# Kernel optimization log

Hardware: AMD Instinct MI355X
Metric: run time of the kernel (lower is better)

## Reference

```python
import jax, jax.numpy as jnp
import numpy as np
from jax.scipy.linalg import cho_solve

N_OBS = 2_000_000
DIM = 16
EPS = 1e-6
LOG_DIM = 32  # module uses self.dim = 32 (param count) in the log-2pi term; faithful to source


def _block_diag_cov(params):
    # params: (32,) -> 8 blocks of 2x2, block = B @ B^T + eps*I, assembled block-diagonally
    B = params.reshape(8, 2, 2)
    blocks = jnp.einsum('nij,nkj->nik', B, B) + EPS * jnp.eye(2, dtype=params.dtype)
    idx = jnp.arange(8)
    M = jnp.zeros((8, 2, 8, 2), dtype=params.dtype).at[idx, :, idx, :].set(blocks)
    return M.reshape(16, 16)


def _transform_mu(mu, pose):
    # interleaved (x,y) points, rotate about centroid, translate to pose[:2]
    pts = jnp.stack([mu[0::2], mu[1::2]])  # (2, 8)
    centroid = jnp.mean(pts, axis=1, keepdims=True)
    ct, st = jnp.cos(pose[2]), jnp.sin(pose[2])
    R = jnp.stack([jnp.stack([ct, -st]), jnp.stack([st, ct])])  # (2,2)
    pts = R @ (pts - centroid) + pose[:2, None]
    return jnp.zeros(16, dtype=mu.dtype).at[0::2].set(pts[0]).at[1::2].set(pts[1])


def setup_inputs() -> dict:
    key = jax.random.key(0)
    k1, k2, k3, k4, k5 = jax.random.split(key, 5)
    obs = jax.random.normal(k1, (N_OBS, DIM), dtype=jnp.float32)
    mu_likelihood = jax.random.normal(k2, (DIM,), dtype=jnp.float32)
    # pose init ~ [uniform(15,25), uniform(15,25), uniform(-pi/16, pi/16)]
    u = jax.random.uniform(k3, (3,), dtype=jnp.float32)
    mu_prior_pose = jnp.array([15.0, 15.0, -np.pi / 16], jnp.float32) + u * jnp.array([10.0, 10.0, 2 * np.pi / 16], jnp.float32)
    # covariance params ~ uniform(cov_min=0.01, cov_max=10)
    Sigma_prior_params = jax.random.uniform(k4, (32,), dtype=jnp.float32, minval=0.01, maxval=10.0)
    Sigma_likelihood_params = jax.random.uniform(k5, (32,), dtype=jnp.float32, minval=0.01, maxval=10.0)
    return {
        'obs': obs,
        'mu_likelihood': mu_likelihood,
        'mu_prior_pose': mu_prior_pose,
        'Sigma_prior_params': Sigma_prior_params,
        'Sigma_likelihood_params': Sigma_likelihood_params,
    }


def reference(obs, mu_likelihood, mu_prior_pose, Sigma_prior_params, Sigma_likelihood_params):
    Sigma_prior = _block_diag_cov(Sigma_prior_params)
    Sigma_likelihood = _block_diag_cov(Sigma_likelihood_params)
    eye = jnp.eye(DIM, dtype=jnp.float32)

    L_prior = jnp.linalg.cholesky(Sigma_prior)
    prior_precision = cho_solve((L_prior, True), eye)
    L_like = jnp.linalg.cholesky(Sigma_likelihood)
    like_precision = cho_solve((L_like, True), eye)

    posterior_precision = prior_precision + like_precision
    L_post = jnp.linalg.cholesky(posterior_precision)
    Sigma_post = cho_solve((L_post, True), eye)

    mu_prior = _transform_mu(mu_likelihood, mu_prior_pose)
    mu_post = Sigma_post @ (cho_solve((L_prior, True), mu_prior) + cho_solve((L_like, True), mu_likelihood))

    diff = obs - mu_post  # (N, 16)
    # NOTE: faithful to source, which uses logdet of the *precision* and
    # quad form with Sigma_post = inv(posterior_precision)
    logdet = 2.0 * jnp.sum(jnp.log(jnp.diagonal(L_post)))
    quad = jnp.sum((diff @ Sigma_post) * diff, axis=1)  # (N,)
    log_terms = -0.5 * LOG_DIM * jnp.log(jnp.asarray(2.0 * jnp.pi, jnp.float32)) - 0.5 * logdet - 0.5 * quad
    return -jnp.sum(log_terms)
```

## Files before the change

### kernel.cpp

```cpp
#include <hip/hip_runtime.h>
#include <math.h>

#define EPS_COV 1e-6f
#define NBLOCKS 2048

typedef float vfloat4 __attribute__((ext_vector_type(4)));


__global__ __launch_bounds__(256) void quad_stream_kernel(
    const vfloat4* __restrict__ obs4,
    const float*  __restrict__ mu_like,
    const float*  __restrict__ pose,
    const float*  __restrict__ sp_prior,
    const float*  __restrict__ sp_like,
    double*       __restrict__ partials,
    int n4)
{
    const int tid    = blockIdx.x * blockDim.x + threadIdx.x;
    const int stride = gridDim.x * blockDim.x;
    const int q = tid & 3;

    float cx = 0.f, cy = 0.f;
    #pragma unroll
    for (int i = 0; i < 8; ++i) { cx += mu_like[2*i]; cy += mu_like[2*i+1]; }
    cx *= 0.125f; cy *= 0.125f;
    const float ct = cosf(pose[2]), st = sinf(pose[2]);
    const float tx = pose[0], ty = pose[1];

    float m0=0.f, m1=0.f, m2=0.f, m3=0.f;
    float a0=0.f, b0=0.f, c0=0.f, a1=0.f, b1=0.f, c1=0.f;

    #pragma unroll
    for (int n = 0; n < 8; ++n) {
        float px = mu_like[2*n]   - cx;
        float py = mu_like[2*n+1] - cy;
        float mp0 = ct*px - st*py + tx;
        float mp1 = st*px + ct*py + ty;

        const float* p = sp_prior + 4*n;
        float s00 = p[0]*p[0] + p[1]*p[1] + EPS_COV;
        float s01 = p[0]*p[2] + p[1]*p[3];
        float s11 = p[2]*p[2] + p[3]*p[3] + EPS_COV;
        float det = s00*s11 - s01*s01;
        float Pp00 =  s11/det, Pp01 = -s01/det, Pp11 = s00/det;

        const float* l = sp_like + 4*n;
        float t00 = l[0]*l[0] + l[1]*l[1] + EPS_COV;
        float t01 = l[0]*l[2] + l[1]*l[3];
        float t11 = l[2]*l[2] + l[3]*l[3] + EPS_COV;
        float dl = t00*t11 - t01*t01;
        float Pl00 =  t11/dl, Pl01 = -t01/dl, Pl11 = t00/dl;

        float Q00 = Pp00 + Pl00, Q01 = Pp01 + Pl01, Q11 = Pp11 + Pl11;
        float dq = Q00*Q11 - Q01*Q01;
        float S00 = Q11/dq, S01 = -Q01/dq, S11v = Q00/dq;

        float ml0 = mu_like[2*n], ml1 = mu_like[2*n+1];
        float v0 = Pp00*mp0 + Pp01*mp1 + Pl00*ml0 + Pl01*ml1;
        float v1 = Pp01*mp0 + Pp11*mp1 + Pl01*ml0 + Pl11*ml1;
        float mpostx = S00*v0 + S01*v1;
        float mposty = S01*v0 + S11v*v1;

        if (n == 2*q)     { m0 = mpostx; m1 = mposty; a0 = S00; b0 = 2.f*S01; c0 = S11v; }
        if (n == 2*q + 1) { m2 = mpostx; m3 = mposty; a1 = S00; b1 = 2.f*S01; c1 = S11v; }
    }

    float acc0 = 0.f, acc1 = 0.f;
    int i = tid;
    while (i + 7*stride < n4) {
        vfloat4 v[8];
        #pragma unroll
        for (int j = 0; j < 8; ++j)
            v[j] = __builtin_nontemporal_load(&obs4[i + j*stride]);
        #pragma unroll
        for (int j = 0; j < 8; ++j) {
            float d0 = v[j].x - m0, d1 = v[j].y - m1;
            float d2 = v[j].z - m2, d3 = v[j].w - m3;
            float t = a0*d0*d0 + b0*(d0*d1) + c0*d1*d1
                    + a1*d2*d2 + b1*(d2*d3) + c1*d3*d3;
            if (j & 1) acc1 += t; else acc0 += t;
        }
        i += 8*stride;
    }
    for (; i < n4; i += stride) {
        vfloat4 v = __builtin_nontemporal_load(&obs4[i]);
        float d0 = v.x - m0, d1 = v.y - m1;
        float d2 = v.z - m2, d3 = v.w - m3;
        acc0 += a0*d0*d0 + b0*(d0*d1) + c0*d1*d1
              + a1*d2*d2 + b1*(d2*d3) + c1*d3*d3;
    }

    double accd = (double)acc0 + (double)acc1;

    #pragma unroll
    for (int off = 32; off > 0; off >>= 1)
        accd += __shfl_down(accd, off, 64);

    __shared__ double lds[4];
    const int wave = threadIdx.x >> 6;
    if ((threadIdx.x & 63) == 0) lds[wave] = accd;
    __syncthreads();
    if (threadIdx.x == 0)
        partials[blockIdx.x] = lds[0] + lds[1] + lds[2] + lds[3];
}

__global__ __launch_bounds__(256) void finalize_kernel(
    const double* __restrict__ partials,
    const float*  __restrict__ sp_prior,
    const float*  __restrict__ sp_like,
    float*        __restrict__ out,
    int nblocks, double n_obs)
{
    double s = 0.0;
    for (int i = threadIdx.x; i < nblocks; i += 256) s += partials[i];
    #pragma unroll
    for (int off = 32; off > 0; off >>= 1)
        s += __shfl_down(s, off, 64);
    __shared__ double lds[4];
    const int wave = threadIdx.x >> 6;
    if ((threadIdx.x & 63) == 0) lds[wave] = s;
    __syncthreads();

    if (threadIdx.x == 0) {
        double total = lds[0] + lds[1] + lds[2] + lds[3];
        double logdet = 0.0;
        for (int n = 0; n < 8; ++n) {
            const float* p = sp_prior + 4*n;
            double s00 = (double)p[0]*p[0] + (double)p[1]*p[1] + 1e-6;
            double s01 = (double)p[0]*p[2] + (double)p[1]*p[3];
            double s11 = (double)p[2]*p[2] + (double)p[3]*p[3] + 1e-6;
            double det = s00*s11 - s01*s01;
            double Pp00 = s11/det, Pp01 = -s01/det, Pp11 = s00/det;
            const float* l = sp_like + 4*n;
            double t00 = (double)l[0]*l[0] + (double)l[1]*l[1] + 1e-6;
            double t01 = (double)l[0]*l[2] + (double)l[1]*l[3];
            double t11 = (double)l[2]*l[2] + (double)l[3]*l[3] + 1e-6;
            double dl = t00*t11 - t01*t01;
            double Pl00 = t11/dl, Pl01 = -t01/dl, Pl11 = t00/dl;
            double Q00 = Pp00 + Pl00, Q01 = Pp01 + Pl01, Q11 = Pp11 + Pl11;
            logdet += log(Q00*Q11 - Q01*Q01);
        }
        const double LOG_2PI = 1.8378770664093454835606594728112;
        double c = n_obs * (16.0 * LOG_2PI + 0.5 * logdet);
        out[0] = (float)(c + 0.5 * total);
    }
}

extern "C" void kernel_launch(void* const* d_in, const int* in_sizes, int n_in,
                              void* d_out, int out_size, void* d_ws, size_t ws_size,
                              hipStream_t stream) {
    const float* obs      = (const float*)d_in[0];
    const float* mu_like  = (const float*)d_in[1];
    const float* pose     = (const float*)d_in[2];
    const float* sp_prior = (const float*)d_in[3];
    const float* sp_like  = (const float*)d_in[4];
    float* out = (float*)d_out;

    double* partials = (double*)d_ws;

    const int n_elems  = in_sizes[0];
    const int n4       = n_elems / 4;
    const double n_obs = (double)(n_elems / 16);

    quad_stream_kernel<<<NBLOCKS, 256, 0, stream>>>(
        (const vfloat4*)obs, mu_like, pose, sp_prior, sp_like, partials, n4);

    finalize_kernel<<<1, 256, 0, stream>>>(partials, sp_prior, sp_like, out, NBLOCKS, n_obs);
}
```

Baseline: 194.3 us.

## Fuse streaming reduction and finalize into one cooperative kernel with grid sync

```diff
diff --git a/kernel.cpp b/kernel.cpp
--- a/kernel.cpp
+++ b/kernel.cpp
@@ -1,69 +1,109 @@
 #include <hip/hip_runtime.h>
+#include <hip/hip_cooperative_groups.h>
 #include <math.h>
 
+namespace cg = cooperative_groups;
+
 #define EPS_COV 1e-6f
-#define NBLOCKS 2048
+#define NBLOCKS 1024
+#define NTHREADS 256
 
 typedef float vfloat4 __attribute__((ext_vector_type(4)));
 
 
-__global__ __launch_bounds__(256) void quad_stream_kernel(
+
+__device__ __forceinline__ void setup_params(
+    const float* __restrict__ mu_like, const float* __restrict__ pose,
+    const float* __restrict__ sp_prior, const float* __restrict__ sp_like, int q,
+    float& m0, float& m1, float& m2, float& m3,
+    float& a0, float& b0, float& c0,
+    float& a1, float& b1, float& c1)
+{
+    float cx = 0.f, cy = 0.f;
+    #pragma unroll
+    for (int i = 0; i < 8; ++i) { cx += mu_like[2*i]; cy += mu_like[2*i+1]; }
+    cx *= 0.125f; cy *= 0.125f;
+    const float ct = cosf(pose[2]), st = sinf(pose[2]);
+    const float tx = pose[0], ty = pose[1];
+
+    #pragma unroll
+    for (int k = 0; k < 2; ++k) {
+        const int n = 2*q + k;
+        float px = mu_like[2*n]   - cx;
+        float py = mu_like[2*n+1] - cy;
+        float mp0 = ct*px - st*py + tx;
+        float mp1 = st*px + ct*py + ty;
+
+        const float* p = sp_prior + 4*n;
+        float s00 = p[0]*p[0] + p[1]*p[1] + EPS_COV;
+        float s01 = p[0]*p[2] + p[1]*p[3];
+        float s11 = p[2]*p[2] + p[3]*p[3] + EPS_COV;
+        float det = s00*s11 - s01*s01;
+        float Pp00 =  s11/det, Pp01 = -s01/det, Pp11 = s00/det;
+
+        const float* l = sp_like + 4*n;
+        float t00 = l[0]*l[0] + l[1]*l[1] + EPS_COV;
+        float t01 = l[0]*l[2] + l[1]*l[3];
+        float t11 = l[2]*l[2] + l[3]*l[3] + EPS_COV;
+        float dl = t00*t11 - t01*t01;
+        float Pl00 =  t11/dl, Pl01 = -t01/dl, Pl11 = t00/dl;
+
+        float Q00 = Pp00 + Pl00, Q01 = Pp01 + Pl01, Q11 = Pp11 + Pl11;
+        float dq = Q00*Q11 - Q01*Q01;
+        float S00 = Q11/dq, S01 = -Q01/dq, S11v = Q00/dq;
+
+        float ml0 = mu_like[2*n], ml1 = mu_like[2*n+1];
+        float v0 = Pp00*mp0 + Pp01*mp1 + Pl00*ml0 + Pl01*ml1;
+        float v1 = Pp01*mp0 + Pp11*mp1 + Pl01*ml0 + Pl11*ml1;
+        float mpostx = S00*v0 + S01*v1;
+        float mposty = S01*v0 + S11v*v1;
+
+        if (k == 0) { m0 = mpostx; m1 = mposty; a0 = S00; b0 = 2.f*S01; c0 = S11v; }
+        else        { m2 = mpostx; m3 = mposty; a1 = S00; b1 = 2.f*S01; c1 = S11v; }
+    }
+}
+
+__device__ __forceinline__ double logdet_posterior(
+    const float* __restrict__ sp_prior, const float* __restrict__ sp_like)
+{
+    double logdet = 0.0;
+    for (int n = 0; n < 8; ++n) {
+        const float* p = sp_prior + 4*n;
+        double s00 = (double)p[0]*p[0] + (double)p[1]*p[1] + 1e-6;
+        double s01 = (double)p[0]*p[2] + (double)p[1]*p[3];
+        double s11 = (double)p[2]*p[2] + (double)p[3]*p[3] + 1e-6;
+        double det = s00*s11 - s01*s01;
+        double Pp00 = s11/det, Pp01 = -s01/det, Pp11 = s00/det;
+        const float* l = sp_like + 4*n;
+        double t00 = (double)l[0]*l[0] + (double)l[1]*l[1] + 1e-6;
+        double t01 = (double)l[0]*l[2] + (double)l[1]*l[3];
+        double t11 = (double)l[2]*l[2] + (double)l[3]*l[3] + 1e-6;
+        double dl = t00*t11 - t01*t01;
+        double Pl00 = t11/dl, Pl01 = -t01/dl, Pl11 = t00/dl;
+        double Q00 = Pp00 + Pl00, Q01 = Pp01 + Pl01, Q11 = Pp11 + Pl11;
+        logdet += log(Q00*Q11 - Q01*Q01);
+    }
+    return logdet;
+}
+
+
+__global__ __launch_bounds__(NTHREADS, 4) void fused_quad_kernel(
     const vfloat4* __restrict__ obs4,
     const float*  __restrict__ mu_like,
     const float*  __restrict__ pose,
     const float*  __restrict__ sp_prior,
     const float*  __restrict__ sp_like,
     double*       __restrict__ partials,
-    int n4)
+    float*        __restrict__ out,
+    int n4, double n_obs)
 {
     const int tid    = blockIdx.x * blockDim.x + threadIdx.x;
     const int stride = gridDim.x * blockDim.x;
     const int q = tid & 3;
 
-    float cx = 0.f, cy = 0.f;
-    #pragma unroll
-    for (int i = 0; i < 8; ++i) { cx += mu_like[2*i]; cy += mu_like[2*i+1]; }
-    cx *= 0.125f; cy *= 0.125f;
-    const float ct = cosf(pose[2]), st = sinf(pose[2]);
-    const float tx = pose[0], ty = pose[1];
-
-    float m0=0.f, m1=0.f, m2=0.f, m3=0.f;
-    float a0=0.f, b0=0.f, c0=0.f, a1=0.f, b1=0.f, c1=0.f;
-
-    #pragma unroll
-    for (int n = 0; n < 8; ++n) {
-        float px = mu_like[2*n]   - cx;
-        float py = mu_like[2*n+1] - cy;
-        float mp0 = ct*px - st*py + tx;
-        float mp1 = st*px + ct*py + ty;
-
-        const float* p = sp_prior + 4*n;
-        float s00 = p[0]*p[0] + p[1]*p[1] + EPS_COV;
-        float s01 = p[0]*p[2] + p[1]*p[3];
-        float s11 = p[2]*p[2] + p[3]*p[3] + EPS_COV;
-        float det = s00*s11 - s01*s01;
-        float Pp00 =  s11/det, Pp01 = -s01/det, Pp11 = s00/det;
-
-        const float* l = sp_like + 4*n;
-        float t00 = l[0]*l[0] + l[1]*l[1] + EPS_COV;
-        float t01 = l[0]*l[2] + l[1]*l[3];
-        float t11 = l[2]*l[2] + l[3]*l[3] + EPS_COV;
-        float dl = t00*t11 - t01*t01;
-        float Pl00 =  t11/dl, Pl01 = -t01/dl, Pl11 = t00/dl;
-
-        float Q00 = Pp00 + Pl00, Q01 = Pp01 + Pl01, Q11 = Pp11 + Pl11;
-        float dq = Q00*Q11 - Q01*Q01;
-        float S00 = Q11/dq, S01 = -Q01/dq, S11v = Q00/dq;
-
-        float ml0 = mu_like[2*n], ml1 = mu_like[2*n+1];
-        float v0 = Pp00*mp0 + Pp01*mp1 + Pl00*ml0 + Pl01*ml1;
-        float v1 = Pp01*mp0 + Pp11*mp1 + Pl01*ml0 + Pl11*ml1;
-        float mpostx = S00*v0 + S01*v1;
-        float mposty = S01*v0 + S11v*v1;
-
-        if (n == 2*q)     { m0 = mpostx; m1 = mposty; a0 = S00; b0 = 2.f*S01; c0 = S11v; }
-        if (n == 2*q + 1) { m2 = mpostx; m3 = mposty; a1 = S00; b1 = 2.f*S01; c1 = S11v; }
-    }
+    float m0, m1, m2, m3, a0, b0, c0, a1, b1, c1;
+    setup_params(mu_like, pose, sp_prior, sp_like, q,
+                 m0, m1, m2, m3, a0, b0, c0, a1, b1, c1);
 
     float acc0 = 0.f, acc1 = 0.f;
     int i = tid;
@@ -100,11 +140,91 @@
     const int wave = threadIdx.x >> 6;
     if ((threadIdx.x & 63) == 0) lds[wave] = accd;
     __syncthreads();
+    if (threadIdx.x == 0) {
+        double blocksum = lds[0] + lds[1] + lds[2] + lds[3];
+        __hip_atomic_store(&partials[blockIdx.x], blocksum,
+                           __ATOMIC_RELEASE, __HIP_MEMORY_SCOPE_AGENT);
+    }
+
+    cg::this_grid().sync();
+
+    if (blockIdx.x == 0) {
+        double s = 0.0;
+        for (int k = threadIdx.x; k < NBLOCKS; k += NTHREADS)
+            s += __hip_atomic_load(&partials[k], __ATOMIC_RELAXED,
+                                   __HIP_MEMORY_SCOPE_AGENT);
+        #pragma unroll
+        for (int off = 32; off > 0; off >>= 1)
+            s += __shfl_down(s, off, 64);
+        __syncthreads();
+        if ((threadIdx.x & 63) == 0) lds[wave] = s;
+        __syncthreads();
+        if (threadIdx.x == 0) {
+            double total = lds[0] + lds[1] + lds[2] + lds[3];
+            const double LOG_2PI = 1.8378770664093454835606594728112;
+            double c = n_obs * (16.0 * LOG_2PI + 0.5 * logdet_posterior(sp_prior, sp_like));
+            out[0] = (float)(c + 0.5 * total);
+        }
+    }
+}
+
+
+__global__ __launch_bounds__(NTHREADS) void quad_stream_kernel(
+    const vfloat4* __restrict__ obs4,
+    const float*  __restrict__ mu_like,
+    const float*  __restrict__ pose,
+    const float*  __restrict__ sp_prior,
+    const float*  __restrict__ sp_like,
+    double*       __restrict__ partials,
+    int n4)
+{
+    const int tid    = blockIdx.x * blockDim.x + threadIdx.x;
+    const int stride = gridDim.x * blockDim.x;
+    const int q = tid & 3;
+
+    float m0, m1, m2, m3, a0, b0, c0, a1, b1, c1;
+    setup_params(mu_like, pose, sp_prior, sp_like, q,
+                 m0, m1, m2, m3, a0, b0, c0, a1, b1, c1);
+
+    float acc0 = 0.f, acc1 = 0.f;
+    int i = tid;
+    while (i + 7*stride < n4) {
+        vfloat4 v[8];
+        #pragma unroll
+        for (int j = 0; j < 8; ++j)
+            v[j] = __builtin_nontemporal_load(&obs4[i + j*stride]);
+        #pragma unroll
+        for (int j = 0; j < 8; ++j) {
+            float d0 = v[j].x - m0, d1 = v[j].y - m1;
+            float d2 = v[j].z - m2, d3 = v[j].w - m3;
+            float t = a0*d0*d0 + b0*(d0*d1) + c0*d1*d1
+                    + a1*d2*d2 + b1*(d2*d3) + c1*d3*d3;
+            if (j & 1) acc1 += t; else acc0 += t;
+        }
+        i += 8*stride;
+    }
+    for (; i < n4; i += stride) {
+        vfloat4 v = __builtin_nontemporal_load(&obs4[i]);
+        float d0 = v.x - m0, d1 = v.y - m1;
+        float d2 = v.z - m2, d3 = v.w - m3;
+        acc0 += a0*d0*d0 + b0*(d0*d1) + c0*d1*d1
+              + a1*d2*d2 + b1*(d2*d3) + c1*d3*d3;
+    }
+
+    double accd = (double)acc0 + (double)acc1;
+    #pragma unroll
+    for (int off = 32; off > 0; off >>= 1)
+        accd += __shfl_down(accd, off, 64);
+
+    __shared__ double lds[4];
+    const int wave = threadIdx.x >> 6;
+    if ((threadIdx.x & 63) == 0) lds[wave] = accd;
+    __syncthreads();
     if (threadIdx.x == 0)
         partials[blockIdx.x] = lds[0] + lds[1] + lds[2] + lds[3];
 }
 
-__global__ __launch_bounds__(256) void finalize_kernel(
+__global__ __launch_bounds__(NTHREADS) void finalize_kernel(
     const double* __restrict__ partials,
     const float*  __restrict__ sp_prior,
     const float*  __restrict__ sp_like,
@@ -112,7 +232,7 @@
     int nblocks, double n_obs)
 {
     double s = 0.0;
-    for (int i = threadIdx.x; i < nblocks; i += 256) s += partials[i];
+    for (int i = threadIdx.x; i < nblocks; i += NTHREADS) s += partials[i];
     #pragma unroll
     for (int off = 32; off > 0; off >>= 1)
         s += __shfl_down(s, off, 64);
@@ -123,25 +243,8 @@
 
     if (threadIdx.x == 0) {
         double total = lds[0] + lds[1] + lds[2] + lds[3];
-        double logdet = 0.0;
-        for (int n = 0; n < 8; ++n) {
-            const float* p = sp_prior + 4*n;
-            double s00 = (double)p[0]*p[0] + (double)p[1]*p[1] + 1e-6;
-            double s01 = (double)p[0]*p[2] + (double)p[1]*p[3];
-            double s11 = (double)p[2]*p[2] + (double)p[3]*p[3] + 1e-6;
-            double det = s00*s11 - s01*s01;
-            double Pp00 = s11/det, Pp01 = -s01/det, Pp11 = s00/det;
-            const float* l = sp_like + 4*n;
-            double t00 = (double)l[0]*l[0] + (double)l[1]*l[1] + 1e-6;
-            double t01 = (double)l[0]*l[2] + (double)l[1]*l[3];
-            double t11 = (double)l[2]*l[2] + (double)l[3]*l[3] + 1e-6;
-            double dl = t00*t11 - t01*t01;
-            double Pl00 = t11/dl, Pl01 = -t01/dl, Pl11 = t00/dl;
-            double Q00 = Pp00 + Pl00, Q01 = Pp01 + Pl01, Q11 = Pp11 + Pl11;
-            logdet += log(Q00*Q11 - Q01*Q01);
-        }
         const double LOG_2PI = 1.8378770664093454835606594728112;
-        double c = n_obs * (16.0 * LOG_2PI + 0.5 * logdet);
+        double c = n_obs * (16.0 * LOG_2PI + 0.5 * logdet_posterior(sp_prior, sp_like));
         out[0] = (float)(c + 0.5 * total);
     }
 }
@@ -149,21 +252,29 @@
 extern "C" void kernel_launch(void* const* d_in, const int* in_sizes, int n_in,
                               void* d_out, int out_size, void* d_ws, size_t ws_size,
                               hipStream_t stream) {
-    const float* obs      = (const float*)d_in[0];
+    const vfloat4* obs4   = (const vfloat4*)d_in[0];
     const float* mu_like  = (const float*)d_in[1];
     const float* pose     = (const float*)d_in[2];
     const float* sp_prior = (const float*)d_in[3];
     const float* sp_like  = (const float*)d_in[4];
     float* out = (float*)d_out;
-
     double* partials = (double*)d_ws;
 
-    const int n_elems  = in_sizes[0];
-    const int n4       = n_elems / 4;
-    const double n_obs = (double)(n_elems / 16);
-
-    quad_stream_kernel<<<NBLOCKS, 256, 0, stream>>>(
-        (const vfloat4*)obs, mu_like, pose, sp_prior, sp_like, partials, n4);
-
-    finalize_kernel<<<1, 256, 0, stream>>>(partials, sp_prior, sp_like, out, NBLOCKS, n_obs);
-}
+    int n4 = in_sizes[0] / 4;
+    double n_obs = (double)(in_sizes[0] / 16);
+
+    void* args[] = { (void*)&obs4, (void*)&mu_like, (void*)&pose,
+                     (void*)&sp_prior, (void*)&sp_like,
+                     (void*)&partials, (void*)&out, (void*)&n4, (void*)&n_obs };
+
+    hipError_t err = hipLaunchCooperativeKernel(
+        (const void*)fused_quad_kernel, dim3(NBLOCKS), dim3(NTHREADS),
+        args, 0, stream);
+
+    if (err != hipSuccess) {
+        quad_stream_kernel<<<NBLOCKS, NTHREADS, 0, stream>>>(
+            obs4, mu_like, pose, sp_prior, sp_like, partials, n4);
+        finalize_kernel<<<1, NTHREADS, 0, stream>>>(
+            partials, sp_prior, sp_like, out, NBLOCKS, n_obs);
+    }
+}
```

New measurement: 353.6 us. +82.0%, slower.
